# Performance work log

Hardware: AMD Instinct MI355X
Metric: run time of the kernel (lower is better)

The kernel has to match this reference:

```python
import jax, jax.numpy as jnp
import numpy as np

B, S, D, H = 4, 1024, 1024, 16
E = 8                 # num_experts
FF1 = 4096            # d_hidden * expansion_factor * 2 (swiglu in)
FF2 = 2048            # d_hidden * expansion_factor (swiglu out / linear2 in)
TEMP = 0.5            # gating temperature
RMS_EPS_GATE = float(np.finfo(np.float32).eps)  # torch RMSNorm default eps
NORM_EPS = 1e-8       # layer_norm_eps


def setup_inputs() -> dict:
    key = jax.random.key(0)
    ks = jax.random.split(key, 8)
    s = 0.02
    return {
        "x": jax.random.normal(ks[0], (B, S, D), jnp.float32),
        "w_qkv": jax.random.normal(ks[1], (3 * D, D), jnp.float32) * s,
        "w_out": jax.random.normal(ks[2], (D, D), jnp.float32) * s,
        "norm1_w": jnp.ones((D,), jnp.float32),
        "norm2_w": jnp.ones((D,), jnp.float32),
        "gate_w": jax.random.normal(ks[3], (E, D), jnp.float32) * s,
        "gate_b": jnp.zeros((E,), jnp.float32),
        "gate_rms_w": jnp.ones((E,), jnp.float32),
        "w1": jax.random.normal(ks[4], (E, D, FF1), jnp.float32) * s,
        "w2": jax.random.normal(ks[5], (E, FF2, D), jnp.float32) * s,
    }


def _rmsnorm(x, w, eps):
    return x * w * jax.lax.rsqrt(jnp.mean(x * x, axis=-1, keepdims=True) + eps)


def _attn(h, w_qkv, w_out):
    qkv = h @ w_qkv.T                              # [B,S,3D]
    q, k, v = jnp.split(qkv, 3, axis=-1)
    dh = D // H
    q = q.reshape(B, S, H, dh)
    k = k.reshape(B, S, H, dh)
    v = v.reshape(B, S, H, dh)
    scores = jnp.einsum("bqhd,bkhd->bhqk", q, k) / jnp.sqrt(jnp.float32(dh))
    p = jax.nn.softmax(scores, axis=-1)
    o = jnp.einsum("bhqk,bkhd->bqhd", p, v).reshape(B, S, D)
    return o @ w_out.T


def _moe(h, gate_w, gate_b, gate_rms_w, w1, w2):
    xf = h.reshape(-1, D)                          # [N,D]
    logits = _rmsnorm(xf @ gate_w.T + gate_b, gate_rms_w, RMS_EPS_GATE)
    gates = jax.nn.softmax(logits / TEMP, axis=-1)  # [N,E]
    top_g, _ = jax.lax.top_k(gates, 1)              # top_k = 1
    # capacity dispatch mask degenerates to all-ones (capacity >= 1), so
    # normalized gate = g / (g + 1e-6)
    g = top_g[:, 0] / (top_g[:, 0] + 1e-6)          # [N]
    h1 = jnp.einsum("nd,edf->nef", xf, w1)          # [N,E,FF1]
    a, b = jnp.split(h1, 2, axis=-1)                # SwiGLU
    act = a * jax.nn.silu(b)                        # [N,E,FF2]
    outs = jnp.einsum("nef,efd->ned", act, w2)      # [N,E,D]
    # gate broadcasts over the expert axis (as in the original code)
    comb = outs.sum(axis=1) * g[:, None]
    return comb.reshape(h.shape)


def reference(x, w_qkv, w_out, norm1_w, norm2_w, gate_w, gate_b, gate_rms_w, w1, w2):
    # pre-norm transformer block, eval mode (no dropout / gating noise)
    x = x + _attn(_rmsnorm(x, norm1_w, NORM_EPS), w_qkv, w_out)
    x = x + _moe(_rmsnorm(x, norm2_w, NORM_EPS), gate_w, gate_b, gate_rms_w, w1, w2)
    return x
```

## Files before the change

kernel.cpp:

```cpp
#include <hip/hip_runtime.h>
#include <hip/hip_bf16.h>
#include <math.h>

typedef __bf16 bf16_t;
typedef __bf16 bf16x8 __attribute__((ext_vector_type(8)));
typedef float f32x4 __attribute__((ext_vector_type(4)));

typedef const __attribute__((address_space(1))) void* gptr_t;
typedef __attribute__((address_space(3))) void* lptr_t;

#define MFMA16(a, b, c) __builtin_amdgcn_mfma_f32_16x16x32_bf16((a), (b), (c), 0, 0, 0)
#define BAR() __builtin_amdgcn_s_barrier()
#define WAIT_LGKM()                                        \
  do {                                                     \
    asm volatile("s_waitcnt lgkmcnt(0)" ::: "memory");     \
    __builtin_amdgcn_sched_barrier(0);                     \
  } while (0)
#define WAIT_VM4()                                         \
  do {                                                     \
    asm volatile("s_waitcnt vmcnt(4)" ::: "memory");       \
    __builtin_amdgcn_sched_barrier(0);                     \
  } while (0)
#define WAIT_VM8()                                         \
  do {                                                     \
    asm volatile("s_waitcnt vmcnt(8)" ::: "memory");       \
    __builtin_amdgcn_sched_barrier(0);                     \
  } while (0)
#define WAIT_VM0()                                         \
  do {                                                     \
    asm volatile("s_waitcnt vmcnt(0)" ::: "memory");       \
    __builtin_amdgcn_sched_barrier(0);                     \
  } while (0)

__device__ __forceinline__ void gload_lds16(const bf16_t* g, bf16_t* l) {
  __builtin_amdgcn_global_load_lds((gptr_t)g, (lptr_t)l, 16, 0, 0);
}

__global__ __launch_bounds__(256) void conv_kernel(const float* __restrict__ in,
                                                   bf16_t* __restrict__ out, int n4) {
  int i = blockIdx.x * 256 + threadIdx.x;
  if (i >= n4) return;
  float4 v = ((const float4*)in)[i];
  bf16_t* o = out + (size_t)i * 4;
  o[0] = (bf16_t)v.x; o[1] = (bf16_t)v.y; o[2] = (bf16_t)v.z; o[3] = (bf16_t)v.w;
}

__global__ __launch_bounds__(256) void transp_w1(const float* __restrict__ in,
                                                 bf16_t* __restrict__ out) {
  __shared__ float tile[64][65];
  const float* ip = in + (size_t)blockIdx.z * 1024 * 4096;
  bf16_t* op = out + (size_t)blockIdx.z * 4096 * 1024;
  int t = threadIdx.x;
  int r0 = blockIdx.y * 64, c0 = blockIdx.x * 64;
  int lr = t >> 4, lc4 = (t & 15) * 4;
#pragma unroll
  for (int p = 0; p < 4; ++p) {
    float4 v = *(const float4*)&ip[(size_t)(r0 + p * 16 + lr) * 4096 + c0 + lc4];
    tile[p * 16 + lr][lc4 + 0] = v.x;
    tile[p * 16 + lr][lc4 + 1] = v.y;
    tile[p * 16 + lr][lc4 + 2] = v.z;
    tile[p * 16 + lr][lc4 + 3] = v.w;
  }
  __syncthreads();
  int c = t >> 2, rs = (t & 3) * 16;
  int cg = c0 + c;
  int pc = (cg < 2048) ? ((cg >> 5) * 64 + (cg & 31))
                       : (((cg - 2048) >> 5) * 64 + 32 + ((cg - 2048) & 31));
#pragma unroll
  for (int h = 0; h < 2; ++h) {
    bf16x8 v;
#pragma unroll
    for (int i = 0; i < 8; ++i) v[i] = (bf16_t)tile[rs + h * 8 + i][c];
    *(bf16x8*)&op[(size_t)pc * 1024 + r0 + rs + h * 8] = v;
  }
}

__global__ __launch_bounds__(256) void transp_w2(const float* __restrict__ in,
                                                 bf16_t* __restrict__ out) {
  __shared__ float tile[64][65];
  const float* ip = in + (size_t)blockIdx.z * 2048 * 1024;
  int t = threadIdx.x;
  int r0 = blockIdx.y * 64, c0 = blockIdx.x * 64;
  int lr = t >> 4, lc4 = (t & 15) * 4;
#pragma unroll
  for (int p = 0; p < 4; ++p) {
    float4 v = *(const float4*)&ip[(size_t)(r0 + p * 16 + lr) * 1024 + c0 + lc4];
    tile[p * 16 + lr][lc4 + 0] = v.x;
    tile[p * 16 + lr][lc4 + 1] = v.y;
    tile[p * 16 + lr][lc4 + 2] = v.z;
    tile[p * 16 + lr][lc4 + 3] = v.w;
  }
  __syncthreads();
  int c = t >> 2, rs = (t & 3) * 16;
#pragma unroll
  for (int h = 0; h < 2; ++h) {
    bf16x8 v;
#pragma unroll
    for (int i = 0; i < 8; ++i) v[i] = (bf16_t)tile[rs + h * 8 + i][c];
    *(bf16x8*)&out[(size_t)(c0 + c) * 16384 + blockIdx.z * 2048 + r0 + rs + h * 8] = v;
  }
}

__global__ __launch_bounds__(256) void rmsnorm_kernel(const float* __restrict__ x,
                                                      const float* __restrict__ w,
                                                      bf16_t* __restrict__ out, float eps) {
  int row = blockIdx.x;
  int t = threadIdx.x;
  const float4* xr = (const float4*)(x + (size_t)row * 1024);
  float4 v = xr[t];
  float ss = v.x * v.x + v.y * v.y + v.z * v.z + v.w * v.w;
#pragma unroll
  for (int off = 1; off < 64; off <<= 1) ss += __shfl_xor(ss, off, 64);
  __shared__ float red[4];
  int wave = t >> 6, lane = t & 63;
  if (lane == 0) red[wave] = ss;
  __syncthreads();
  ss = red[0] + red[1] + red[2] + red[3];
  float inv = rsqrtf(ss * (1.0f / 1024.0f) + eps);
  float4 wv = ((const float4*)w)[t];
  bf16_t* o = out + (size_t)row * 1024 + t * 4;
  o[0] = (bf16_t)(v.x * wv.x * inv);
  o[1] = (bf16_t)(v.y * wv.y * inv);
  o[2] = (bf16_t)(v.z * wv.z * inv);
  o[3] = (bf16_t)(v.w * wv.w * inv);
}

template <int EPI>
__global__ __launch_bounds__(512, 2) void gemm256(const bf16_t* __restrict__ A,
                                                  const bf16_t* __restrict__ Bt,
                                                  void* __restrict__ C,
                                                  const float* __restrict__ resid,
                                                  int M, int N, int K, int lda, int ldb) {
  __shared__ bf16_t As[2][256 * 64];
  __shared__ bf16_t Bs[2][256 * 64];
  const int tid = threadIdx.x;
  const int wave = tid >> 6, lane = tid & 63;

  const int gx = gridDim.x, gy = gridDim.y;
  int nwg = gx * gy * gridDim.z;
  int lin = blockIdx.x + gx * (blockIdx.y + gy * blockIdx.z);
  int wid = ((nwg & 7) == 0) ? ((lin & 7) * (nwg >> 3) + (lin >> 3)) : lin;
  int bx, by, bz;
  if (EPI == 4 && gx == 16 && gy == 16 && gridDim.z == 8) {
    int local = wid & 255;
    int st = local >> 4, wi = local & 15;
    bx = (st & 3) * 4 + (wi & 3);
    by = (st >> 2) * 4 + (wi >> 2);
    bz = wid >> 8;
  } else {
    bx = wid % gx;
    by = (wid / gx) % gy;
    bz = wid / (gx * gy);
  }

  const int m0 = by * 256, n0 = bx * 256;
  const int wr = (wave >> 2) * 128, wc = (wave & 3) * 64;
  const int fr = lane & 15, fq = lane >> 4;

  if (EPI == 4) Bt += (size_t)bz * 4096 * 1024;
  if (EPI == 5) {
    A += (size_t)bz * K;
    Bt += (size_t)bz * K;
  }

  const int srw = lane >> 3;
  const int sgc = (lane & 7) ^ srw;
  const bf16_t* aBase = A + (size_t)(m0 + wave * 8 + srw) * lda + sgc * 8;
  const bf16_t* bBase = Bt + (size_t)(n0 + wave * 8 + srw) * ldb + sgc * 8;

  auto stageA = [&](bf16_t* buf, int kt) {
#pragma unroll
    for (int i = 0; i < 4; ++i) {
      int r = i * 64;
      gload_lds16(aBase + (size_t)r * lda + kt * 64, &buf[(r + wave * 8) * 64]);
    }
  };
  auto stageB = [&](bf16_t* buf, int kt) {
#pragma unroll
    for (int i = 0; i < 4; ++i) {
      int r = i * 64;
      gload_lds16(bBase + (size_t)r * ldb + kt * 64, &buf[(r + wave * 8) * 64]);
    }
  };

  f32x4 acc[8][4] = {};
  bf16x8 a_[4][2], b_[4][2];

  auto readA = [&](int b, int mh) {
#pragma unroll
    for (int q = 0; q < 4; ++q)
#pragma unroll
      for (int ks = 0; ks < 2; ++ks) {
        int r = wr + mh * 64 + q * 16 + fr;
        a_[q][ks] = *(const bf16x8*)&As[b][r * 64 + (((fq + ks * 4) ^ (fr & 7)) << 3)];
      }
  };
  auto readB = [&](int b, int nh) {
#pragma unroll
    for (int q = 0; q < 2; ++q)
#pragma unroll
      for (int ks = 0; ks < 2; ++ks) {
        int r = wc + nh * 32 + q * 16 + fr;
        b_[nh * 2 + q][ks] = *(const bf16x8*)&Bs[b][r * 64 + (((fq + ks * 4) ^ (fr & 7)) << 3)];
      }
  };
  auto mfma16x = [&](int mh, int nh) {
    __builtin_amdgcn_s_setprio(1);
#pragma unroll
    for (int q = 0; q < 4; ++q)
#pragma unroll
      for (int n = 0; n < 2; ++n)
#pragma unroll
        for (int ks = 0; ks < 2; ++ks)
          acc[mh * 4 + q][nh * 2 + n] =
              MFMA16(a_[q][ks], b_[nh * 2 + n][ks], acc[mh * 4 + q][nh * 2 + n]);
    __builtin_amdgcn_s_setprio(0);
  };

  const int NKT = K >> 6;
  stageB(Bs[0], 0);
  stageA(As[0], 0);
  stageB(Bs[1], 1);
  stageA(As[1], 1);
  WAIT_VM8();
  BAR();
  readA(0, 0);
  readB(0, 0);

  for (int it = 0; it < (NKT >> 1) - 1; ++it) {
    const int t2 = 2 * it + 2, t3 = 2 * it + 3;
    WAIT_LGKM(); mfma16x(0, 0); readB(0, 1); BAR();
    WAIT_LGKM(); mfma16x(0, 1); readA(0, 1); BAR();
    WAIT_LGKM(); mfma16x(1, 0); stageB(Bs[0], t2); WAIT_VM4(); BAR();
    WAIT_LGKM(); mfma16x(1, 1); readA(1, 0); readB(1, 0); stageA(As[0], t2); BAR();
    WAIT_LGKM(); mfma16x(0, 0); readB(1, 1); BAR();
    WAIT_LGKM(); mfma16x(0, 1); readA(1, 1); BAR();
    WAIT_LGKM(); mfma16x(1, 0); stageB(Bs[1], t3); WAIT_VM4(); BAR();
    WAIT_LGKM(); mfma16x(1, 1); readA(0, 0); readB(0, 0); stageA(As[1], t3); BAR();
  }

  WAIT_LGKM(); mfma16x(0, 0); readB(0, 1); BAR();
  WAIT_LGKM(); mfma16x(0, 1); readA(0, 1); BAR();
  WAIT_LGKM(); mfma16x(1, 0); WAIT_VM0(); BAR();
  WAIT_LGKM(); mfma16x(1, 1); readA(1, 0); readB(1, 0); BAR();
  WAIT_LGKM(); mfma16x(0, 0); readB(1, 1); BAR();
  WAIT_LGKM(); mfma16x(0, 1); readA(1, 1); BAR();
  WAIT_LGKM(); mfma16x(1, 0); BAR();
  WAIT_LGKM(); mfma16x(1, 1);

  if (EPI == 4) {
    bf16_t* act = (bf16_t*)C;
    int strip = (n0 >> 6) + (wave & 3);
#pragma unroll
    for (int mq = 0; mq < 8; ++mq)
#pragma unroll
      for (int n = 0; n < 2; ++n)
#pragma unroll
        for (int j = 0; j < 4; ++j) {
          size_t row = (size_t)(m0 + wr + mq * 16 + fq * 4 + j);
          size_t col = (size_t)bz * 2048 + strip * 32 + n * 16 + fr;
          float a = acc[mq][n][j], b = acc[mq][n + 2][j];
          act[row * 16384 + col] = (bf16_t)(a * (b / (1.0f + __expf(-b))));
        }
    return;
  }
#pragma unroll
  for (int mq = 0; mq < 8; ++mq)
#pragma unroll
    for (int n = 0; n < 4; ++n)
#pragma unroll
      for (int j = 0; j < 4; ++j) {
        size_t row = (size_t)(m0 + wr + mq * 16 + fq * 4 + j);
        size_t col = (size_t)(n0 + wc + n * 16 + fr);
        float v = acc[mq][n][j];
        if (EPI == 0)
          ((bf16_t*)C)[row * N + col] = (bf16_t)v;
        else if (EPI == 1)
          ((float*)C)[row * N + col] = resid[row * N + col] + v;
        else if (EPI == 5)
          ((float*)C + (size_t)bz * M * N)[row * N + col] = v;
      }
}

__global__ __launch_bounds__(512) void attn_kernel(const bf16_t* __restrict__ qkv,
                                                   bf16_t* __restrict__ o) {
  const int S = 1024, LD = 3072;
  int qt = blockIdx.x, bh = blockIdx.y;
  int b = bh >> 4, h = bh & 15;
  int tid = threadIdx.x, wave = tid >> 6, lane = tid & 63;
  int fr = lane & 15, fq = lane >> 4, kg = fq * 8;
  int q0 = qt * 128 + wave * 16;
  const bf16_t* qb = qkv + (size_t)b * S * LD + h * 64;
  const bf16_t* kb = qb + 1024;
  const bf16_t* vb = qb + 2048;

  __shared__ bf16_t Ks[64 * 64];
  __shared__ bf16_t Vt[64 * 64];
  __shared__ bf16_t Ps[8][16 * 72];

  bf16x8 qf0 = *(const bf16x8*)&qb[(size_t)(q0 + fr) * LD + kg];
  bf16x8 qf1 = *(const bf16x8*)&qb[(size_t)(q0 + fr) * LD + 32 + kg];

  f32x4 acc[4] = {};
  float mrow[4] = {-1e30f, -1e30f, -1e30f, -1e30f};
  float ssum[4] = {0.f, 0.f, 0.f, 0.f};

  for (int k0 = 0; k0 < S; k0 += 64) {
    {
      int c = tid;
      int r = c >> 3, ch = c & 7;
      *(bf16x8*)&Ks[r * 64 + ((ch ^ (r & 7)) << 3)] =
          *(const bf16x8*)&kb[(size_t)(k0 + r) * LD + ch * 8];
      bf16x8 vv = *(const bf16x8*)&vb[(size_t)(k0 + r) * LD + ch * 8];
#pragma unroll
      for (int i = 0; i < 8; ++i) {
        int d = ch * 8 + i;
        int cs = ((r >> 3) ^ (d >> 3) ^ (d & 7)) & 7;
        Vt[d * 64 + cs * 8 + (r & 7)] = vv[i];
      }
    }
    __syncthreads();

    f32x4 s[4];
#pragma unroll
    for (int kc = 0; kc < 4; ++kc) {
      int row = kc * 16 + fr, sw = row & 7;
      bf16x8 kf0 = *(const bf16x8*)&Ks[row * 64 + ((fq ^ sw) << 3)];
      bf16x8 kf1 = *(const bf16x8*)&Ks[row * 64 + (((4 + fq) ^ sw) << 3)];
      f32x4 z = {};
      z = MFMA16(qf0, kf0, z);
      z = MFMA16(qf1, kf1, z);
      s[kc] = z * 0.125f;
    }
    float pmax[4], psum[4], scl[4];
#pragma unroll
    for (int j = 0; j < 4; ++j)
      pmax[j] = fmaxf(fmaxf(s[0][j], s[1][j]), fmaxf(s[2][j], s[3][j]));
#pragma unroll
    for (int off = 1; off < 16; off <<= 1)
#pragma unroll
      for (int j = 0; j < 4; ++j) pmax[j] = fmaxf(pmax[j], __shfl_xor(pmax[j], off, 64));
#pragma unroll
    for (int j = 0; j < 4; ++j) {
      float nm = fmaxf(mrow[j], pmax[j]);
      scl[j] = __expf(mrow[j] - nm);
      mrow[j] = nm;
      psum[j] = 0.f;
    }
#pragma unroll
    for (int kc = 0; kc < 4; ++kc)
#pragma unroll
      for (int j = 0; j < 4; ++j) {
        float p = __expf(s[kc][j] - mrow[j]);
        psum[j] += p;
        Ps[wave][(fq * 4 + j) * 72 + kc * 16 + fr] = (bf16_t)p;
      }
#pragma unroll
    for (int off = 1; off < 16; off <<= 1)
#pragma unroll
      for (int j = 0; j < 4; ++j) psum[j] += __shfl_xor(psum[j], off, 64);
#pragma unroll
    for (int j = 0; j < 4; ++j) ssum[j] = ssum[j] * scl[j] + psum[j];
#pragma unroll
    for (int n = 0; n < 4; ++n)
#pragma unroll
      for (int j = 0; j < 4; ++j) acc[n][j] *= scl[j];
    asm volatile("s_waitcnt lgkmcnt(0)" ::: "memory");
    bf16x8 pa[2];
#pragma unroll
    for (int ks = 0; ks < 2; ++ks) pa[ks] = *(const bf16x8*)&Ps[wave][fr * 72 + ks * 32 + kg];
#pragma unroll
    for (int n = 0; n < 4; ++n) {
      int d = n * 16 + fr;
      int swd = ((d >> 3) ^ (d & 7)) & 7;
#pragma unroll
      for (int ks = 0; ks < 2; ++ks) {
        bf16x8 vbf = *(const bf16x8*)&Vt[d * 64 + (((ks * 4 + fq) ^ swd) << 3)];
        acc[n] = MFMA16(pa[ks], vbf, acc[n]);
      }
    }
    __syncthreads();
  }
#pragma unroll
  for (int n = 0; n < 4; ++n)
#pragma unroll
    for (int j = 0; j < 4; ++j) {
      size_t row = (size_t)b * S + q0 + fq * 4 + j;
      o[row * 1024 + h * 64 + n * 16 + fr] = (bf16_t)(acc[n][j] / ssum[j]);
    }
}

__global__ __launch_bounds__(256) void gate_kernel(const bf16_t* __restrict__ hn,
                                                   const float* __restrict__ gw,
                                                   const float* __restrict__ gb,
                                                   const float* __restrict__ grms,
                                                   float* __restrict__ g) {
  int n = blockIdx.x * 4 + (threadIdx.x >> 6);
  int lane = threadIdx.x & 63;
  const bf16_t* xr = hn + (size_t)n * 1024;
  float acc[8] = {};
  for (int i = lane; i < 1024; i += 64) {
    float xv = (float)xr[i];
#pragma unroll
    for (int e = 0; e < 8; ++e) acc[e] += xv * gw[e * 1024 + i];
  }
#pragma unroll
  for (int e = 0; e < 8; ++e)
    for (int off = 1; off < 64; off <<= 1) acc[e] += __shfl_xor(acc[e], off, 64);
  float l[8], ms = 0.f;
#pragma unroll
  for (int e = 0; e < 8; ++e) {
    l[e] = acc[e] + gb[e];
    ms += l[e] * l[e];
  }
  float inv = rsqrtf(ms * 0.125f + 1.1920928955078125e-07f);
  float mx = -1e30f;
#pragma unroll
  for (int e = 0; e < 8; ++e) {
    l[e] = l[e] * inv * grms[e] * 2.0f;
    mx = fmaxf(mx, l[e]);
  }
  float s = 0.f;
#pragma unroll
  for (int e = 0; e < 8; ++e) s += __expf(l[e] - mx);
  float t = 1.0f / s;
  if (lane == 0) g[n] = t / (t + 1e-6f);
}

__global__ __launch_bounds__(256) void combine4(const float* __restrict__ moep,
                                                const float* __restrict__ x1,
                                                const float* __restrict__ g,
                                                float* __restrict__ out, int Mc) {
  size_t i4 = (size_t)blockIdx.x * 256 + threadIdx.x;
  size_t row = i4 >> 8;
  size_t stride4 = (size_t)Mc * 256;
  float4 s = {0.f, 0.f, 0.f, 0.f};
#pragma unroll
  for (int z = 0; z < 4; ++z) {
    float4 v = ((const float4*)moep)[z * stride4 + i4];
    s.x += v.x; s.y += v.y; s.z += v.z; s.w += v.w;
  }
  float gv = g[row];
  float4 xv = ((const float4*)x1)[i4];
  float4 r;
  r.x = xv.x + s.x * gv;
  r.y = xv.y + s.y * gv;
  r.z = xv.z + s.z * gv;
  r.w = xv.w + s.w * gv;
  ((float4*)out)[i4] = r;
}

extern "C" void kernel_launch(void* const* d_in, const int* in_sizes, int n_in,
                              void* d_out, int out_size, void* d_ws, size_t ws_size,
                              hipStream_t stream) {
  const float* x = (const float*)d_in[0];
  const float* w_qkv = (const float*)d_in[1];
  const float* w_out = (const float*)d_in[2];
  const float* norm1_w = (const float*)d_in[3];
  const float* norm2_w = (const float*)d_in[4];
  const float* gate_w = (const float*)d_in[5];
  const float* gate_b = (const float*)d_in[6];
  const float* gate_rms = (const float*)d_in[7];
  const float* w1 = (const float*)d_in[8];
  const float* w2 = (const float*)d_in[9];
  float* out = (float*)d_out;

  const size_t baseB = (8ull * 4096 * 1024 + 1024ull * 16384 + 3072ull * 1024 +
                        1024ull * 1024 + 4096ull * 1024) * 2 +
                       4096ull * 1024 * 4 + 4096 * 4;
  int cc = 4;
  if (ws_size >= baseB + 4096ull * 16384 * 2 + 4ull * 4096 * 1024 * 4)
    cc = 1;
  else if (ws_size >= baseB + 2048ull * 16384 * 2 + 4ull * 2048 * 1024 * 4)
    cc = 2;
  const int Mc = 4096 / cc;

  char* ws = (char*)d_ws;
  size_t off = 0;
  auto alloc = [&](size_t bytes) {
    char* p = ws + off;
    off += bytes;
    return p;
  };
  bf16_t* w1t = (bf16_t*)alloc(8ull * 4096 * 1024 * 2);
  bf16_t* w2t = (bf16_t*)alloc(1024ull * 16384 * 2);
  bf16_t* wqkvb = (bf16_t*)alloc(3072ull * 1024 * 2);
  bf16_t* woutb = (bf16_t*)alloc(1024ull * 1024 * 2);
  bf16_t* hn = (bf16_t*)alloc(4096ull * 1024 * 2);
  float* x1 = (float*)alloc(4096ull * 1024 * 4);
  float* gbuf = (float*)alloc(4096ull * 4);
  bf16_t* act = (bf16_t*)alloc((size_t)Mc * 16384 * 2);
  float* moep = (float*)alloc(4ull * Mc * 1024 * 4);
  bf16_t* qkvb = (bf16_t*)act;
  bf16_t* attno = (bf16_t*)moep;

  conv_kernel<<<3072, 256, 0, stream>>>(w_qkv, wqkvb, 3072 * 1024 / 4);
  conv_kernel<<<1024, 256, 0, stream>>>(w_out, woutb, 1024 * 1024 / 4);
  transp_w1<<<dim3(64, 16, 8), 256, 0, stream>>>(w1, w1t);
  transp_w2<<<dim3(16, 32, 8), 256, 0, stream>>>(w2, w2t);

  rmsnorm_kernel<<<4096, 256, 0, stream>>>(x, norm1_w, hn, 1e-8f);
  gemm256<0><<<dim3(12, 16), 512, 0, stream>>>(hn, wqkvb, qkvb, nullptr, 4096, 3072, 1024,
                                               1024, 1024);
  attn_kernel<<<dim3(8, 64), 512, 0, stream>>>(qkvb, attno);
  gemm256<1><<<dim3(4, 16), 512, 0, stream>>>(attno, woutb, x1, x, 4096, 1024, 1024, 1024,
                                              1024);

  rmsnorm_kernel<<<4096, 256, 0, stream>>>(x1, norm2_w, hn, 1e-8f);
  gate_kernel<<<1024, 256, 0, stream>>>(hn, gate_w, gate_b, gate_rms, gbuf);
  for (int c = 0; c < cc; ++c) {
    gemm256<4><<<dim3(16, Mc / 256, 8), 512, 0, stream>>>(
        hn + (size_t)c * Mc * 1024, w1t, act, nullptr, Mc, 4096, 1024, 1024, 1024);
    gemm256<5><<<dim3(4, Mc / 256, 4), 512, 0, stream>>>(
        act, w2t, moep, nullptr, Mc, 1024, 4096, 16384, 16384);
    combine4<<<Mc, 256, 0, stream>>>(moep, x1 + (size_t)c * Mc * 1024, gbuf + (size_t)c * Mc,
                                     out + (size_t)c * Mc * 1024, Mc);
  }
}
```

Measured before the change: 601.3 us.

## Shrink GEMM tiles to 256x128x32 with triple-buffered LDS and higher occupancy

The shared GEMM kernel changes from 256x256 tiles with a 64-deep K step and a double-buffered 8-phase schedule to 256x128 tiles with a 32-deep K step. Staging now uses a three-slot LDS ring, with one vmcnt wait per K step. Each wave accumulates a 64x64 block, and launch bounds allow 4 blocks per CU. All launch grids double in N and the EPI4 block swizzle is adjusted to match. The goal is more concurrent blocks, lower register and LDS pressure per block, and better latency hiding. The cost is less data reuse per tile, more barriers per unit of K, and possible off-by-one risks in the three-stage loop bounds.

```diff
diff --git a/kernel.cpp b/kernel.cpp
--- a/kernel.cpp
+++ b/kernel.cpp
@@ -16,14 +16,9 @@
     asm volatile("s_waitcnt lgkmcnt(0)" ::: "memory");     \
     __builtin_amdgcn_sched_barrier(0);                     \
   } while (0)
-#define WAIT_VM4()                                         \
+#define WAIT_VM3()                                         \
   do {                                                     \
-    asm volatile("s_waitcnt vmcnt(4)" ::: "memory");       \
-    __builtin_amdgcn_sched_barrier(0);                     \
-  } while (0)
-#define WAIT_VM8()                                         \
-  do {                                                     \
-    asm volatile("s_waitcnt vmcnt(8)" ::: "memory");       \
+    asm volatile("s_waitcnt vmcnt(3)" ::: "memory");       \
     __builtin_amdgcn_sched_barrier(0);                     \
   } while (0)
 #define WAIT_VM0()                                         \
@@ -126,13 +121,13 @@
 }
 
 template <int EPI>
-__global__ __launch_bounds__(512, 2) void gemm256(const bf16_t* __restrict__ A,
+__global__ __launch_bounds__(512, 4) void gemm256(const bf16_t* __restrict__ A,
                                                   const bf16_t* __restrict__ Bt,
                                                   void* __restrict__ C,
                                                   const float* __restrict__ resid,
                                                   int M, int N, int K, int lda, int ldb) {
-  __shared__ bf16_t As[2][256 * 64];
-  __shared__ bf16_t Bs[2][256 * 64];
+  __shared__ bf16_t As[3][256 * 32];
+  __shared__ bf16_t Bs[3][128 * 32];
   const int tid = threadIdx.x;
   const int wave = tid >> 6, lane = tid & 63;
 
@@ -141,20 +136,20 @@
   int lin = blockIdx.x + gx * (blockIdx.y + gy * blockIdx.z);
   int wid = ((nwg & 7) == 0) ? ((lin & 7) * (nwg >> 3) + (lin >> 3)) : lin;
   int bx, by, bz;
-  if (EPI == 4 && gx == 16 && gy == 16 && gridDim.z == 8) {
-    int local = wid & 255;
+  if (EPI == 4 && gx == 32 && gy == 16 && gridDim.z == 8) {
+    int local = wid & 511;
     int st = local >> 4, wi = local & 15;
-    bx = (st & 3) * 4 + (wi & 3);
-    by = (st >> 2) * 4 + (wi >> 2);
-    bz = wid >> 8;
+    bx = (st & 7) * 4 + (wi & 3);
+    by = (st >> 3) * 4 + (wi >> 2);
+    bz = wid >> 9;
   } else {
     bx = wid % gx;
     by = (wid / gx) % gy;
     bz = wid / (gx * gy);
   }
 
-  const int m0 = by * 256, n0 = bx * 256;
-  const int wr = (wave >> 2) * 128, wc = (wave & 3) * 64;
+  const int m0 = by * 256, n0 = bx * 128;
+  const int wr = (wave >> 1) * 64, wc = (wave & 1) * 64;
   const int fr = lane & 15, fq = lane >> 4;
 
   if (EPI == 4) Bt += (size_t)bz * 4096 * 1024;
@@ -163,116 +158,80 @@
     Bt += (size_t)bz * K;
   }
 
-  const int srw = lane >> 3;
-  const int sgc = (lane & 7) ^ srw;
-  const bf16_t* aBase = A + (size_t)(m0 + wave * 8 + srw) * lda + sgc * 8;
-  const bf16_t* bBase = Bt + (size_t)(n0 + wave * 8 + srw) * ldb + sgc * 8;
-
-  auto stageA = [&](bf16_t* buf, int kt) {
-#pragma unroll
-    for (int i = 0; i < 4; ++i) {
-      int r = i * 64;
-      gload_lds16(aBase + (size_t)r * lda + kt * 64, &buf[(r + wave * 8) * 64]);
-    }
+  const int srow = wave * 16 + (lane >> 2);
+  const int skc = ((lane & 3) ^ ((lane >> 3) & 3)) * 8;
+  const bf16_t* aSrc = A + (size_t)(m0 + srow) * lda + skc;
+  const bf16_t* bSrc = Bt + (size_t)(n0 + srow) * ldb + skc;
+  const int aDst0 = (wave * 16) * 32;
+  const int aDst1 = (128 + wave * 16) * 32;
+
+  auto stage = [&](int buf, int kt) {
+    gload_lds16(aSrc + (size_t)kt * 32, &As[buf][aDst0]);
+    gload_lds16(aSrc + (size_t)128 * lda + (size_t)kt * 32, &As[buf][aDst1]);
+    gload_lds16(bSrc + (size_t)kt * 32, &Bs[buf][aDst0]);
   };
-  auto stageB = [&](bf16_t* buf, int kt) {
-#pragma unroll
-    for (int i = 0; i < 4; ++i) {
-      int r = i * 64;
-      gload_lds16(bBase + (size_t)r * ldb + kt * 64, &buf[(r + wave * 8) * 64]);
-    }
+
+  f32x4 acc[4][4] = {};
+  bf16x8 a_[4], b_[4];
+  const int rch = (fq ^ ((fr >> 1) & 3)) * 8;
+
+  auto readAB = [&](int buf) {
+    const bf16_t* ap = &As[buf][(wr + fr) * 32 + rch];
+#pragma unroll
+    for (int q = 0; q < 4; ++q) a_[q] = *(const bf16x8*)(ap + q * 512);
+    const bf16_t* bp = &Bs[buf][(wc + fr) * 32 + rch];
+#pragma unroll
+    for (int n = 0; n < 4; ++n) b_[n] = *(const bf16x8*)(bp + n * 512);
   };
-
-  f32x4 acc[8][4] = {};
-  bf16x8 a_[4][2], b_[4][2];
-
-  auto readA = [&](int b, int mh) {
+  auto domfma = [&]() {
+    __builtin_amdgcn_s_setprio(1);
 #pragma unroll
     for (int q = 0; q < 4; ++q)
 #pragma unroll
-      for (int ks = 0; ks < 2; ++ks) {
-        int r = wr + mh * 64 + q * 16 + fr;
-        a_[q][ks] = *(const bf16x8*)&As[b][r * 64 + (((fq + ks * 4) ^ (fr & 7)) << 3)];
-      }
-  };
-  auto readB = [&](int b, int nh) {
-#pragma unroll
-    for (int q = 0; q < 2; ++q)
-#pragma unroll
-      for (int ks = 0; ks < 2; ++ks) {
-        int r = wc + nh * 32 + q * 16 + fr;
-        b_[nh * 2 + q][ks] = *(const bf16x8*)&Bs[b][r * 64 + (((fq + ks * 4) ^ (fr & 7)) << 3)];
-      }
-  };
-  auto mfma16x = [&](int mh, int nh) {
-    __builtin_amdgcn_s_setprio(1);
-#pragma unroll
-    for (int q = 0; q < 4; ++q)
-#pragma unroll
-      for (int n = 0; n < 2; ++n)
-#pragma unroll
-        for (int ks = 0; ks < 2; ++ks)
-          acc[mh * 4 + q][nh * 2 + n] =
-              MFMA16(a_[q][ks], b_[nh * 2 + n][ks], acc[mh * 4 + q][nh * 2 + n]);
+      for (int n = 0; n < 4; ++n) acc[q][n] = MFMA16(a_[q], b_[n], acc[q][n]);
     __builtin_amdgcn_s_setprio(0);
   };
 
-  const int NKT = K >> 6;
-  stageB(Bs[0], 0);
-  stageA(As[0], 0);
-  stageB(Bs[1], 1);
-  stageA(As[1], 1);
-  WAIT_VM8();
+  const int NT = K >> 5;
+  stage(0, 0);
+  stage(1, 1);
+  WAIT_VM3();
   BAR();
-  readA(0, 0);
-  readB(0, 0);
-
-  for (int it = 0; it < (NKT >> 1) - 1; ++it) {
-    const int t2 = 2 * it + 2, t3 = 2 * it + 3;
-    WAIT_LGKM(); mfma16x(0, 0); readB(0, 1); BAR();
-    WAIT_LGKM(); mfma16x(0, 1); readA(0, 1); BAR();
-    WAIT_LGKM(); mfma16x(1, 0); stageB(Bs[0], t2); WAIT_VM4(); BAR();
-    WAIT_LGKM(); mfma16x(1, 1); readA(1, 0); readB(1, 0); stageA(As[0], t2); BAR();
-    WAIT_LGKM(); mfma16x(0, 0); readB(1, 1); BAR();
-    WAIT_LGKM(); mfma16x(0, 1); readA(1, 1); BAR();
-    WAIT_LGKM(); mfma16x(1, 0); stageB(Bs[1], t3); WAIT_VM4(); BAR();
-    WAIT_LGKM(); mfma16x(1, 1); readA(0, 0); readB(0, 0); stageA(As[1], t3); BAR();
-  }
-
-  WAIT_LGKM(); mfma16x(0, 0); readB(0, 1); BAR();
-  WAIT_LGKM(); mfma16x(0, 1); readA(0, 1); BAR();
-  WAIT_LGKM(); mfma16x(1, 0); WAIT_VM0(); BAR();
-  WAIT_LGKM(); mfma16x(1, 1); readA(1, 0); readB(1, 0); BAR();
-  WAIT_LGKM(); mfma16x(0, 0); readB(1, 1); BAR();
-  WAIT_LGKM(); mfma16x(0, 1); readA(1, 1); BAR();
-  WAIT_LGKM(); mfma16x(1, 0); BAR();
-  WAIT_LGKM(); mfma16x(1, 1);
+
+  for (int it = 0; it < (NT - 2) / 3; ++it) {
+    const int t = 3 * it;
+    readAB(0); WAIT_LGKM(); domfma(); stage(2, t + 2); WAIT_VM3(); BAR();
+    readAB(1); WAIT_LGKM(); domfma(); stage(0, t + 3); WAIT_VM3(); BAR();
+    readAB(2); WAIT_LGKM(); domfma(); stage(1, t + 4); WAIT_VM3(); BAR();
+  }
+  readAB(0); WAIT_LGKM(); domfma(); WAIT_VM0(); BAR();
+  readAB(1); WAIT_LGKM(); domfma();
 
   if (EPI == 4) {
     bf16_t* act = (bf16_t*)C;
-    int strip = (n0 >> 6) + (wave & 3);
-#pragma unroll
-    for (int mq = 0; mq < 8; ++mq)
+    int strip = bx * 2 + (wave & 1);
+#pragma unroll
+    for (int q = 0; q < 4; ++q)
 #pragma unroll
       for (int n = 0; n < 2; ++n)
 #pragma unroll
         for (int j = 0; j < 4; ++j) {
-          size_t row = (size_t)(m0 + wr + mq * 16 + fq * 4 + j);
+          size_t row = (size_t)(m0 + wr + q * 16 + fq * 4 + j);
           size_t col = (size_t)bz * 2048 + strip * 32 + n * 16 + fr;
-          float a = acc[mq][n][j], b = acc[mq][n + 2][j];
+          float a = acc[q][n][j], b = acc[q][n + 2][j];
           act[row * 16384 + col] = (bf16_t)(a * (b / (1.0f + __expf(-b))));
         }
     return;
   }
 #pragma unroll
-  for (int mq = 0; mq < 8; ++mq)
+  for (int q = 0; q < 4; ++q)
 #pragma unroll
     for (int n = 0; n < 4; ++n)
 #pragma unroll
       for (int j = 0; j < 4; ++j) {
-        size_t row = (size_t)(m0 + wr + mq * 16 + fq * 4 + j);
+        size_t row = (size_t)(m0 + wr + q * 16 + fq * 4 + j);
         size_t col = (size_t)(n0 + wc + n * 16 + fr);
-        float v = acc[mq][n][j];
+        float v = acc[q][n][j];
         if (EPI == 0)
           ((bf16_t*)C)[row * N + col] = (bf16_t)v;
         else if (EPI == 1)
@@ -500,18 +459,18 @@
   transp_w2<<<dim3(16, 32, 8), 256, 0, stream>>>(w2, w2t);
 
   rmsnorm_kernel<<<4096, 256, 0, stream>>>(x, norm1_w, hn, 1e-8f);
-  gemm256<0><<<dim3(12, 16), 512, 0, stream>>>(hn, wqkvb, qkvb, nullptr, 4096, 3072, 1024,
+  gemm256<0><<<dim3(24, 16), 512, 0, stream>>>(hn, wqkvb, qkvb, nullptr, 4096, 3072, 1024,
                                                1024, 1024);
   attn_kernel<<<dim3(8, 64), 512, 0, stream>>>(qkvb, attno);
-  gemm256<1><<<dim3(4, 16), 512, 0, stream>>>(attno, woutb, x1, x, 4096, 1024, 1024, 1024,
+  gemm256<1><<<dim3(8, 16), 512, 0, stream>>>(attno, woutb, x1, x, 4096, 1024, 1024, 1024,
                                               1024);
 
   rmsnorm_kernel<<<4096, 256, 0, stream>>>(x1, norm2_w, hn, 1e-8f);
   gate_kernel<<<1024, 256, 0, stream>>>(hn, gate_w, gate_b, gate_rms, gbuf);
   for (int c = 0; c < cc; ++c) {
-    gemm256<4><<<dim3(16, Mc / 256, 8), 512, 0, stream>>>(
+    gemm256<4><<<dim3(32, Mc / 256, 8), 512, 0, stream>>>(
         hn + (size_t)c * Mc * 1024, w1t, act, nullptr, Mc, 4096, 1024, 1024, 1024);
-    gemm256<5><<<dim3(4, Mc / 256, 4), 512, 0, stream>>>(
+    gemm256<5><<<dim3(8, Mc / 256, 4), 512, 0, stream>>>(
         act, w2t, moep, nullptr, Mc, 1024, 4096, 16384, 16384);
     combine4<<<Mc, 256, 0, stream>>>(moep, x1 + (size_t)c * Mc * 1024, gbuf + (size_t)c * Mc,
                                      out + (size_t)c * Mc * 1024, Mc);
```

Result: slower. 642.2 us (+6.8%).

## Reschedule GEMM main loop with half-tile staggered global-to-LDS loads

Applied to the files above, without the earlier changes.

Splits each A/B tile stage into two half-tile global_load_lds groups and interleaves them across the eight MFMA phases, so global loads are spread more evenly through the k-loop. LDS reads now come before each MFMA block, with barriers on both sides of it. The aim is to smooth memory issue and overlap it better with compute. In exchange the loop has twice as many barriers per phase, and the tighter vmcnt/buffer reuse ordering risks stalls or races.

```diff
diff --git a/kernel.cpp b/kernel.cpp
--- a/kernel.cpp
+++ b/kernel.cpp
@@ -19,11 +19,6 @@
 #define WAIT_VM4()                                         \
   do {                                                     \
     asm volatile("s_waitcnt vmcnt(4)" ::: "memory");       \
-    __builtin_amdgcn_sched_barrier(0);                     \
-  } while (0)
-#define WAIT_VM8()                                         \
-  do {                                                     \
-    asm volatile("s_waitcnt vmcnt(8)" ::: "memory");       \
     __builtin_amdgcn_sched_barrier(0);                     \
   } while (0)
 #define WAIT_VM0()                                         \
@@ -168,19 +163,15 @@
   const bf16_t* aBase = A + (size_t)(m0 + wave * 8 + srw) * lda + sgc * 8;
   const bf16_t* bBase = Bt + (size_t)(n0 + wave * 8 + srw) * ldb + sgc * 8;
 
-  auto stageA = [&](bf16_t* buf, int kt) {
-#pragma unroll
-    for (int i = 0; i < 4; ++i) {
-      int r = i * 64;
-      gload_lds16(aBase + (size_t)r * lda + kt * 64, &buf[(r + wave * 8) * 64]);
-    }
+  auto stageA = [&](int buf, int kt, int h) {
+    gload_lds16(aBase + (size_t)(h * 128) * lda + kt * 64, &As[buf][(h * 128 + wave * 8) * 64]);
+    gload_lds16(aBase + (size_t)(h * 128 + 64) * lda + kt * 64,
+                &As[buf][(h * 128 + 64 + wave * 8) * 64]);
   };
-  auto stageB = [&](bf16_t* buf, int kt) {
-#pragma unroll
-    for (int i = 0; i < 4; ++i) {
-      int r = i * 64;
-      gload_lds16(bBase + (size_t)r * ldb + kt * 64, &buf[(r + wave * 8) * 64]);
-    }
+  auto stageB = [&](int buf, int kt, int h) {
+    gload_lds16(bBase + (size_t)(h * 128) * ldb + kt * 64, &Bs[buf][(h * 128 + wave * 8) * 64]);
+    gload_lds16(bBase + (size_t)(h * 128 + 64) * ldb + kt * 64,
+                &Bs[buf][(h * 128 + 64 + wave * 8) * 64]);
   };
 
   f32x4 acc[8][4] = {};
@@ -218,35 +209,50 @@
   };
 
   const int NKT = K >> 6;
-  stageB(Bs[0], 0);
-  stageA(As[0], 0);
-  stageB(Bs[1], 1);
-  stageA(As[1], 1);
-  WAIT_VM8();
+  stageB(0, 0, 0); stageB(0, 0, 1);
+  stageA(0, 0, 0); stageA(0, 0, 1);
+  stageB(1, 1, 0); stageB(1, 1, 1);
+  WAIT_VM4();
   BAR();
-  readA(0, 0);
-  readB(0, 0);
 
   for (int it = 0; it < (NKT >> 1) - 1; ++it) {
-    const int t2 = 2 * it + 2, t3 = 2 * it + 3;
-    WAIT_LGKM(); mfma16x(0, 0); readB(0, 1); BAR();
-    WAIT_LGKM(); mfma16x(0, 1); readA(0, 1); BAR();
-    WAIT_LGKM(); mfma16x(1, 0); stageB(Bs[0], t2); WAIT_VM4(); BAR();
-    WAIT_LGKM(); mfma16x(1, 1); readA(1, 0); readB(1, 0); stageA(As[0], t2); BAR();
-    WAIT_LGKM(); mfma16x(0, 0); readB(1, 1); BAR();
-    WAIT_LGKM(); mfma16x(0, 1); readA(1, 1); BAR();
-    WAIT_LGKM(); mfma16x(1, 0); stageB(Bs[1], t3); WAIT_VM4(); BAR();
-    WAIT_LGKM(); mfma16x(1, 1); readA(0, 0); readB(0, 0); stageA(As[1], t3); BAR();
-  }
-
-  WAIT_LGKM(); mfma16x(0, 0); readB(0, 1); BAR();
-  WAIT_LGKM(); mfma16x(0, 1); readA(0, 1); BAR();
-  WAIT_LGKM(); mfma16x(1, 0); WAIT_VM0(); BAR();
-  WAIT_LGKM(); mfma16x(1, 1); readA(1, 0); readB(1, 0); BAR();
-  WAIT_LGKM(); mfma16x(0, 0); readB(1, 1); BAR();
-  WAIT_LGKM(); mfma16x(0, 1); readA(1, 1); BAR();
-  WAIT_LGKM(); mfma16x(1, 0); BAR();
-  WAIT_LGKM(); mfma16x(1, 1);
+    const int t1 = 2 * it + 1, t2 = 2 * it + 2, t3 = 2 * it + 3;
+    readA(0, 0); readB(0, 0); stageA(1, t1, 0);
+    BAR(); WAIT_LGKM(); mfma16x(0, 0); BAR();
+    readB(0, 1); stageA(1, t1, 1);
+    BAR(); WAIT_LGKM(); mfma16x(0, 1); BAR();
+    readA(0, 1); stageB(0, t2, 0);
+    BAR(); WAIT_LGKM(); mfma16x(1, 0); BAR();
+    stageB(0, t2, 1); WAIT_VM4();
+    BAR(); mfma16x(1, 1); BAR();
+    readA(1, 0); readB(1, 0); stageA(0, t2, 0);
+    BAR(); WAIT_LGKM(); mfma16x(0, 0); BAR();
+    readB(1, 1); stageA(0, t2, 1);
+    BAR(); WAIT_LGKM(); mfma16x(0, 1); BAR();
+    readA(1, 1); stageB(1, t3, 0);
+    BAR(); WAIT_LGKM(); mfma16x(1, 0); BAR();
+    stageB(1, t3, 1); WAIT_VM4();
+    BAR(); mfma16x(1, 1); BAR();
+  }
+
+  {
+    const int t1 = NKT - 1;
+    readA(0, 0); readB(0, 0); stageA(1, t1, 0);
+    BAR(); WAIT_LGKM(); mfma16x(0, 0); BAR();
+    readB(0, 1); stageA(1, t1, 1);
+    BAR(); WAIT_LGKM(); mfma16x(0, 1); BAR();
+    readA(0, 1);
+    BAR(); WAIT_LGKM(); mfma16x(1, 0); BAR();
+    WAIT_VM0();
+    BAR(); mfma16x(1, 1); BAR();
+    readA(1, 0); readB(1, 0);
+    BAR(); WAIT_LGKM(); mfma16x(0, 0); BAR();
+    readB(1, 1);
+    BAR(); WAIT_LGKM(); mfma16x(0, 1); BAR();
+    readA(1, 1);
+    BAR(); WAIT_LGKM(); mfma16x(1, 0); BAR();
+    mfma16x(1, 1);
+  }
 
   if (EPI == 4) {
     bf16_t* act = (bf16_t*)C;
```

New measurement: 641.6 us. 6.7% more time.

## Switch GEMM to 32x32x16 MFMA and prefetch attention K/V tiles into registers

Applied to the files above, without the earlier changes.

The main GEMM kernel now uses 32x32x16 bf16 MFMA instructions instead of 16x16x32, with fragment layouts, LDS reads and epilogue index maps rewritten to match. Larger MFMA tiles cut instruction count and LDS read traffic per FLOP. Separately, the attention kernel loads the next K/V tile into registers right after the barrier, so global latency overlaps with compute. The risks are higher accumulator register pressure, possible LDS bank conflicts under the new swizzled read pattern, and a missing barrier before Ks/Vt are overwritten on the next iteration.

```diff
diff --git a/kernel.cpp b/kernel.cpp
--- a/kernel.cpp
+++ b/kernel.cpp
@@ -5,11 +5,13 @@
 typedef __bf16 bf16_t;
 typedef __bf16 bf16x8 __attribute__((ext_vector_type(8)));
 typedef float f32x4 __attribute__((ext_vector_type(4)));
+typedef float f32x16 __attribute__((ext_vector_type(16)));
 
 typedef const __attribute__((address_space(1))) void* gptr_t;
 typedef __attribute__((address_space(3))) void* lptr_t;
 
 #define MFMA16(a, b, c) __builtin_amdgcn_mfma_f32_16x16x32_bf16((a), (b), (c), 0, 0, 0)
+#define MFMA32(a, b, c) __builtin_amdgcn_mfma_f32_32x32x16_bf16((a), (b), (c), 0, 0, 0)
 #define BAR() __builtin_amdgcn_s_barrier()
 #define WAIT_LGKM()                                        \
   do {                                                     \
@@ -155,7 +157,7 @@
 
   const int m0 = by * 256, n0 = bx * 256;
   const int wr = (wave >> 2) * 128, wc = (wave & 3) * 64;
-  const int fr = lane & 15, fq = lane >> 4;
+  const int l31 = lane & 31, l5 = lane >> 5;
 
   if (EPI == 4) Bt += (size_t)bz * 4096 * 1024;
   if (EPI == 5) {
@@ -183,37 +185,32 @@
     }
   };
 
-  f32x4 acc[8][4] = {};
-  bf16x8 a_[4][2], b_[4][2];
+  f32x16 acc[4][2] = {};
+  bf16x8 a_[2][4], b_[2][4];
 
   auto readA = [&](int b, int mh) {
 #pragma unroll
-    for (int q = 0; q < 4; ++q)
-#pragma unroll
-      for (int ks = 0; ks < 2; ++ks) {
-        int r = wr + mh * 64 + q * 16 + fr;
-        a_[q][ks] = *(const bf16x8*)&As[b][r * 64 + (((fq + ks * 4) ^ (fr & 7)) << 3)];
+    for (int qq = 0; qq < 2; ++qq)
+#pragma unroll
+      for (int ks = 0; ks < 4; ++ks) {
+        int r = wr + mh * 64 + qq * 32 + l31;
+        a_[qq][ks] = *(const bf16x8*)&As[b][r * 64 + (((ks * 2 + l5) ^ (r & 7)) << 3)];
       }
   };
   auto readB = [&](int b, int nh) {
 #pragma unroll
-    for (int q = 0; q < 2; ++q)
-#pragma unroll
-      for (int ks = 0; ks < 2; ++ks) {
-        int r = wc + nh * 32 + q * 16 + fr;
-        b_[nh * 2 + q][ks] = *(const bf16x8*)&Bs[b][r * 64 + (((fq + ks * 4) ^ (fr & 7)) << 3)];
-      }
+    for (int ks = 0; ks < 4; ++ks) {
+      int r = wc + nh * 32 + l31;
+      b_[nh][ks] = *(const bf16x8*)&Bs[b][r * 64 + (((ks * 2 + l5) ^ (r & 7)) << 3)];
+    }
   };
-  auto mfma16x = [&](int mh, int nh) {
+  auto mfmaQ = [&](int mh, int nh) {
     __builtin_amdgcn_s_setprio(1);
 #pragma unroll
-    for (int q = 0; q < 4; ++q)
-#pragma unroll
-      for (int n = 0; n < 2; ++n)
-#pragma unroll
-        for (int ks = 0; ks < 2; ++ks)
-          acc[mh * 4 + q][nh * 2 + n] =
-              MFMA16(a_[q][ks], b_[nh * 2 + n][ks], acc[mh * 4 + q][nh * 2 + n]);
+    for (int qq = 0; qq < 2; ++qq)
+#pragma unroll
+      for (int ks = 0; ks < 4; ++ks)
+        acc[mh * 2 + qq][nh] = MFMA32(a_[qq][ks], b_[nh][ks], acc[mh * 2 + qq][nh]);
     __builtin_amdgcn_s_setprio(0);
   };
 
@@ -229,50 +226,48 @@
 
   for (int it = 0; it < (NKT >> 1) - 1; ++it) {
     const int t2 = 2 * it + 2, t3 = 2 * it + 3;
-    WAIT_LGKM(); mfma16x(0, 0); readB(0, 1); BAR();
-    WAIT_LGKM(); mfma16x(0, 1); readA(0, 1); BAR();
-    WAIT_LGKM(); mfma16x(1, 0); stageB(Bs[0], t2); WAIT_VM4(); BAR();
-    WAIT_LGKM(); mfma16x(1, 1); readA(1, 0); readB(1, 0); stageA(As[0], t2); BAR();
-    WAIT_LGKM(); mfma16x(0, 0); readB(1, 1); BAR();
-    WAIT_LGKM(); mfma16x(0, 1); readA(1, 1); BAR();
-    WAIT_LGKM(); mfma16x(1, 0); stageB(Bs[1], t3); WAIT_VM4(); BAR();
-    WAIT_LGKM(); mfma16x(1, 1); readA(0, 0); readB(0, 0); stageA(As[1], t3); BAR();
-  }
-
-  WAIT_LGKM(); mfma16x(0, 0); readB(0, 1); BAR();
-  WAIT_LGKM(); mfma16x(0, 1); readA(0, 1); BAR();
-  WAIT_LGKM(); mfma16x(1, 0); WAIT_VM0(); BAR();
-  WAIT_LGKM(); mfma16x(1, 1); readA(1, 0); readB(1, 0); BAR();
-  WAIT_LGKM(); mfma16x(0, 0); readB(1, 1); BAR();
-  WAIT_LGKM(); mfma16x(0, 1); readA(1, 1); BAR();
-  WAIT_LGKM(); mfma16x(1, 0); BAR();
-  WAIT_LGKM(); mfma16x(1, 1);
+    WAIT_LGKM(); mfmaQ(0, 0); readB(0, 1); BAR();
+    WAIT_LGKM(); mfmaQ(0, 1); readA(0, 1); BAR();
+    WAIT_LGKM(); mfmaQ(1, 0); stageB(Bs[0], t2); WAIT_VM4(); BAR();
+    WAIT_LGKM(); mfmaQ(1, 1); readA(1, 0); readB(1, 0); stageA(As[0], t2); BAR();
+    WAIT_LGKM(); mfmaQ(0, 0); readB(1, 1); BAR();
+    WAIT_LGKM(); mfmaQ(0, 1); readA(1, 1); BAR();
+    WAIT_LGKM(); mfmaQ(1, 0); stageB(Bs[1], t3); WAIT_VM4(); BAR();
+    WAIT_LGKM(); mfmaQ(1, 1); readA(0, 0); readB(0, 0); stageA(As[1], t3); BAR();
+  }
+
+  WAIT_LGKM(); mfmaQ(0, 0); readB(0, 1); BAR();
+  WAIT_LGKM(); mfmaQ(0, 1); readA(0, 1); BAR();
+  WAIT_LGKM(); mfmaQ(1, 0); WAIT_VM0(); BAR();
+  WAIT_LGKM(); mfmaQ(1, 1); readA(1, 0); readB(1, 0); BAR();
+  WAIT_LGKM(); mfmaQ(0, 0); readB(1, 1); BAR();
+  WAIT_LGKM(); mfmaQ(0, 1); readA(1, 1); BAR();
+  WAIT_LGKM(); mfmaQ(1, 0); BAR();
+  WAIT_LGKM(); mfmaQ(1, 1);
 
   if (EPI == 4) {
     bf16_t* act = (bf16_t*)C;
     int strip = (n0 >> 6) + (wave & 3);
 #pragma unroll
-    for (int mq = 0; mq < 8; ++mq)
-#pragma unroll
-      for (int n = 0; n < 2; ++n)
-#pragma unroll
-        for (int j = 0; j < 4; ++j) {
-          size_t row = (size_t)(m0 + wr + mq * 16 + fq * 4 + j);
-          size_t col = (size_t)bz * 2048 + strip * 32 + n * 16 + fr;
-          float a = acc[mq][n][j], b = acc[mq][n + 2][j];
-          act[row * 16384 + col] = (bf16_t)(a * (b / (1.0f + __expf(-b))));
-        }
+    for (int q = 0; q < 4; ++q)
+#pragma unroll
+      for (int j = 0; j < 16; ++j) {
+        size_t row = (size_t)(m0 + wr + q * 32 + (j & 3) + 8 * (j >> 2) + 4 * l5);
+        size_t col = (size_t)bz * 2048 + strip * 32 + l31;
+        float a = acc[q][0][j], b = acc[q][1][j];
+        act[row * 16384 + col] = (bf16_t)(a * (b / (1.0f + __expf(-b))));
+      }
     return;
   }
 #pragma unroll
-  for (int mq = 0; mq < 8; ++mq)
-#pragma unroll
-    for (int n = 0; n < 4; ++n)
-#pragma unroll
-      for (int j = 0; j < 4; ++j) {
-        size_t row = (size_t)(m0 + wr + mq * 16 + fq * 4 + j);
-        size_t col = (size_t)(n0 + wc + n * 16 + fr);
-        float v = acc[mq][n][j];
+  for (int q = 0; q < 4; ++q)
+#pragma unroll
+    for (int n = 0; n < 2; ++n)
+#pragma unroll
+      for (int j = 0; j < 16; ++j) {
+        size_t row = (size_t)(m0 + wr + q * 32 + (j & 3) + 8 * (j >> 2) + 4 * l5);
+        size_t col = (size_t)(n0 + wc + n * 32 + l31);
+        float v = acc[q][n][j];
         if (EPI == 0)
           ((bf16_t*)C)[row * N + col] = (bf16_t)v;
         else if (EPI == 1)
@@ -305,21 +300,25 @@
   float mrow[4] = {-1e30f, -1e30f, -1e30f, -1e30f};
   float ssum[4] = {0.f, 0.f, 0.f, 0.f};
 
+  int sr = tid >> 3, sch = tid & 7;
+  const bf16_t* krow = kb + (size_t)sr * LD + sch * 8;
+  const bf16_t* vrow = vb + (size_t)sr * LD + sch * 8;
+  bf16x8 kreg = *(const bf16x8*)krow;
+  bf16x8 vreg = *(const bf16x8*)vrow;
+
   for (int k0 = 0; k0 < S; k0 += 64) {
-    {
-      int c = tid;
-      int r = c >> 3, ch = c & 7;
-      *(bf16x8*)&Ks[r * 64 + ((ch ^ (r & 7)) << 3)] =
-          *(const bf16x8*)&kb[(size_t)(k0 + r) * LD + ch * 8];
-      bf16x8 vv = *(const bf16x8*)&vb[(size_t)(k0 + r) * LD + ch * 8];
-#pragma unroll
-      for (int i = 0; i < 8; ++i) {
-        int d = ch * 8 + i;
-        int cs = ((r >> 3) ^ (d >> 3) ^ (d & 7)) & 7;
-        Vt[d * 64 + cs * 8 + (r & 7)] = vv[i];
-      }
+    *(bf16x8*)&Ks[sr * 64 + ((sch ^ (sr & 7)) << 3)] = kreg;
+#pragma unroll
+    for (int i = 0; i < 8; ++i) {
+      int d = sch * 8 + i;
+      int cs = ((sr >> 3) ^ (d >> 3) ^ (d & 7)) & 7;
+      Vt[d * 64 + cs * 8 + (sr & 7)] = vreg[i];
     }
     __syncthreads();
+    if (k0 + 64 < S) {
+      kreg = *(const bf16x8*)(krow + (size_t)(k0 + 64) * LD);
+      vreg = *(const bf16x8*)(vrow + (size_t)(k0 + 64) * LD);
+    }
 
     f32x4 s[4];
 #pragma unroll
```

Measured after the change: 627.5 us, median of 2. 4.4% more time.
